# Performance work log

Hardware: AMD Instinct MI355X
Metric: run time of the kernel (lower is better)

Reference implementation:

```python
import jax, jax.numpy as jnp
import numpy as np

B, N, P = 8, 4096, 1024
P4 = P // 4
EPS = 1e-5


def _ln(x, g, b):
    mu = jnp.mean(x, axis=-1, keepdims=True)
    var = jnp.var(x, axis=-1, keepdims=True)
    return (x - mu) * jax.lax.rsqrt(var + EPS) * g + b


def setup_inputs() -> dict:
    key = jax.random.key(0)
    ks = jax.random.split(key, 16)
    s = lambda fan: 1.0 / np.sqrt(fan)
    return {
        "xyz": jax.random.normal(ks[0], (B, N, 3), jnp.float32),
        "x": jax.random.normal(ks[1], (B, N, P), jnp.float32),
        "ln1_g": jnp.ones((P,), jnp.float32),
        "ln1_b": jnp.zeros((P,), jnp.float32),
        "ln2_g": jnp.ones((P,), jnp.float32),
        "ln2_b": jnp.zeros((P,), jnp.float32),
        "qk_w": jax.random.normal(ks[2], (P4, P), jnp.float32) * s(P),   # shared q/k 1x1 conv, no bias
        "v_w": jax.random.normal(ks[3], (P, P), jnp.float32) * s(P),
        "v_b": jax.random.normal(ks[4], (P,), jnp.float32) * s(P),
        "t1_w": jax.random.normal(ks[5], (P, P4), jnp.float32) * s(P4),  # trans_conv
        "t1_b": jax.random.normal(ks[6], (P,), jnp.float32) * s(P4),
        "t2_w": jax.random.normal(ks[7], (P, P4), jnp.float32) * s(P4),  # trans_conv1
        "t2_b": jax.random.normal(ks[8], (P,), jnp.float32) * s(P4),
        "m1_w": jax.random.normal(ks[9], (P, P), jnp.float32) * s(P),
        "m1_b": jax.random.normal(ks[10], (P,), jnp.float32) * s(P),
        "m2_w": jax.random.normal(ks[11], (P, P), jnp.float32) * s(P),
        "m2_b": jax.random.normal(ks[12], (P,), jnp.float32) * s(P),
    }


def reference(xyz, x, ln1_g, ln1_b, ln2_g, ln2_b, qk_w, v_w, v_b,
              t1_w, t1_b, t2_w, t2_b, m1_w, m1_b, m2_w, m2_b):
    # xyz is accepted but unused, matching the torch module. Dropout = eval identity.
    res1 = x
    h = _ln(x, ln1_g, ln1_b)                                   # [B,N,P]
    # TransformerBlock_1 (1x1 convs on h^T [B,P,N] are just matmuls over P)
    x_q = jnp.einsum('op,bnp->bon', qk_w, h)                   # [B,P4,N]
    # k shares weights with q; x_k permuted is x_q transposed
    x_v = jnp.einsum('op,bnp->bno', v_w, h) + v_b              # [B,N,P]
    energy = jnp.einsum('bqn,bkn->bqk', x_q, x_q)              # [B,P4,P4]
    att = jnp.einsum('op,bpk->bok', t1_w, energy) + t1_b[:, None]   # [B,P,P4]
    att = jax.nn.gelu(att, approximate=False)
    att = jnp.einsum('op,bkp->bok', t2_w, att) + t2_b[:, None]      # [B,P,P]
    att = jax.nn.softmax(att, axis=-1)
    t_out = jnp.einsum('bnp,bpq->bnq', x_v, att)               # [B,N,P]
    x1 = t_out + res1
    h2 = _ln(x1, ln2_g, ln2_b)
    m = jax.nn.gelu(h2 @ m1_w.T + m1_b, approximate=False)
    m = m @ m2_w.T + m2_b
    return x1 + m
```

## Files before the change

### kernel.cpp

```cpp
#include <hip/hip_runtime.h>


typedef __attribute__((ext_vector_type(4))) float f32x4;
typedef __attribute__((ext_vector_type(8))) _Float16 h16x8;
typedef __attribute__((ext_vector_type(8))) unsigned short u16x8;
typedef __attribute__((ext_vector_type(4))) unsigned short u16x4;

__device__ __forceinline__ unsigned short f2h(float f) {
  _Float16 h = (_Float16)f;
  return __builtin_bit_cast(unsigned short, h);
}
__device__ __forceinline__ unsigned split16(float f) {
  _Float16 h = (_Float16)f;
  _Float16 l = (_Float16)(f - (float)h);
  return (unsigned)__builtin_bit_cast(unsigned short, h) |
         ((unsigned)__builtin_bit_cast(unsigned short, l) << 16);
}
__device__ __forceinline__ float gelu_f(float x) {
  return 0.5f * x * (1.0f + erff(x * 0.70710678118654752f));
}
__device__ __forceinline__ void gload16(const void* g, void* l) {
  __builtin_amdgcn_global_load_lds(
      (const __attribute__((address_space(1))) unsigned int*)g,
      (__attribute__((address_space(3))) unsigned int*)l, 16, 0, 0);
}

__global__ __launch_bounds__(256)
void ln_kernel(const float* __restrict__ x, const float* __restrict__ g,
               const float* __restrict__ b, unsigned short* __restrict__ hi,
               unsigned short* __restrict__ lo) {
  __shared__ float red[16];
  const size_t base = (size_t)blockIdx.x * 1024;
  const int t = threadIdx.x;
  f32x4 v = *(const f32x4*)&x[base + t * 4];
  float s = v[0] + v[1] + v[2] + v[3];
  float q = v[0] * v[0] + v[1] * v[1] + v[2] * v[2] + v[3] * v[3];
#pragma unroll
  for (int o = 32; o > 0; o >>= 1) { s += __shfl_down(s, o); q += __shfl_down(q, o); }
  const int w = t >> 6;
  if ((t & 63) == 0) { red[w] = s; red[8 + w] = q; }
  __syncthreads();
  s = (red[0] + red[1]) + (red[2] + red[3]);
  q = (red[8] + red[9]) + (red[10] + red[11]);
  const float mu = s * (1.0f / 1024.0f);
  const float var = q * (1.0f / 1024.0f) - mu * mu;
  const float is = rsqrtf(var + 1e-5f);
  f32x4 gg = *(const f32x4*)&g[t * 4];
  f32x4 bb = *(const f32x4*)&b[t * 4];
  u16x4 oh, ol;
#pragma unroll
  for (int j = 0; j < 4; j++) {
    float y = (v[j] - mu) * is * gg[j] + bb[j];
    unsigned p = split16(y);
    oh[j] = (unsigned short)(p & 0xffffu);
    ol[j] = (unsigned short)(p >> 16);
  }
  *(u16x4*)&hi[base + t * 4] = oh;
  if (lo) *(u16x4*)&lo[base + t * 4] = ol;
}

__global__ __launch_bounds__(256)
void cvt_kernel(const float* __restrict__ in, unsigned short* __restrict__ hi,
                unsigned short* __restrict__ lo, int n4) {
  int i = blockIdx.x * 256 + threadIdx.x;
  if (i < n4) {
    f32x4 v = *(const f32x4*)&in[(size_t)i * 4];
    u16x4 oh, ol;
#pragma unroll
    for (int j = 0; j < 4; j++) {
      unsigned p = split16(v[j]);
      oh[j] = (unsigned short)(p & 0xffffu);
      ol[j] = (unsigned short)(p >> 16);
    }
    *(u16x4*)&hi[(size_t)i * 4] = oh;
    if (lo) *(u16x4*)&lo[(size_t)i * 4] = ol;
  }
}

template <int EPI, int SPLIT>
__global__ __launch_bounds__(256)
void gemm16(const unsigned short* __restrict__ Ahi, const unsigned short* __restrict__ Alo,
            const unsigned short* __restrict__ Bhi, const unsigned short* __restrict__ Blo,
            void* __restrict__ Cout, unsigned short* __restrict__ Cout2,
            const float* __restrict__ bias, const float* __restrict__ resIn,
            int K, int lda, int ldb, int ldc,
            long long sA, long long sB, long long sC, long long sRes, int splitK) {
  __shared__ short As[16384];
  __shared__ short Bs[16384];
  const int z = blockIdx.z;
  const int bi = z / splitK, sp = z % splitK;
  const int kLen = K / splitK, kStart = sp * kLen;
  const unsigned short* AH = Ahi + (size_t)bi * sA;
  const unsigned short* BH = Bhi + (size_t)bi * sB;
  const unsigned short* AL = SPLIT ? Alo + (size_t)bi * sA : nullptr;
  const unsigned short* BL = SPLIT ? Blo + (size_t)bi * sB : nullptr;

  int bx = blockIdx.x, by = blockIdx.y;
  {
    const int nwg = gridDim.x * gridDim.y;
    if ((nwg & 7) == 0 && nwg >= 16) {
      const int flat = bx + gridDim.x * by;
      const int chunk = nwg >> 3;
      const int nf = (flat & 7) * chunk + (flat >> 3);
      bx = nf % gridDim.x;
      by = nf / gridDim.x;
    }
  }
  const int mBase = by * 128, nBase = bx * 128;
  const int t = threadIdx.x, w = t >> 6, l = t & 63;
  const int r16 = l & 15, kq = l >> 4;
  const int wr = (w >> 1) * 64, wc = (w & 1) * 64;
  f32x4 acc[4][4] = {};

  auto stage_hi = [&](int buf, int k0) {
#pragma unroll
    for (int it = 0; it < 4; ++it) {
      const int c = it * 256 + t;
      const int row = c >> 3, cc = c & 7;
      const int gc = cc ^ (row & 7);
      const int cbase = it * 256 + w * 64;
      gload16(&AH[(size_t)(mBase + row) * lda + k0 + gc * 8], &As[buf * 8192 + cbase * 8]);
      gload16(&BH[(size_t)(nBase + row) * ldb + k0 + gc * 8], &Bs[buf * 8192 + cbase * 8]);
    }
  };

  if constexpr (!SPLIT) {
    const int nt = kLen >> 6;
    stage_hi(0, kStart);
    asm volatile("s_waitcnt vmcnt(0)" ::: "memory");
    __syncthreads();
    int cur = 0;
    for (int ts = 0; ts < nt; ++ts) {
      if (ts + 1 < nt) stage_hi(cur ^ 1, kStart + (ts + 1) * 64);
#pragma unroll
      for (int kk = 0; kk < 2; ++kk) {
        h16x8 aH[4], bH[4];
#pragma unroll
        for (int mi = 0; mi < 4; mi++) {
          const int r = wr + mi * 16 + r16;
          const int cc = (kk * 4 + kq) ^ (r & 7);
          aH[mi] = *(const h16x8*)&As[cur * 8192 + r * 64 + cc * 8];
        }
#pragma unroll
        for (int ni = 0; ni < 4; ni++) {
          const int r = wc + ni * 16 + r16;
          const int cc = (kk * 4 + kq) ^ (r & 7);
          bH[ni] = *(const h16x8*)&Bs[cur * 8192 + r * 64 + cc * 8];
        }
#pragma unroll
        for (int mi = 0; mi < 4; mi++)
#pragma unroll
          for (int ni = 0; ni < 4; ni++)
            acc[mi][ni] = __builtin_amdgcn_mfma_f32_16x16x32_f16(aH[mi], bH[ni], acc[mi][ni], 0, 0, 0);
      }
      asm volatile("s_waitcnt vmcnt(0)" ::: "memory");
      __syncthreads();
      cur ^= 1;
    }
  } else {
    for (int k0 = kStart; k0 < kStart + kLen; k0 += 64) {
#pragma unroll
      for (int it = 0; it < 4; ++it) {
        const int c = it * 256 + t;
        const int row = c >> 3, cc = c & 7;
        const int gc = cc ^ (row & 7);
        const int cbase = it * 256 + w * 64;
        const size_t ga = (size_t)(mBase + row) * lda + k0 + gc * 8;
        const size_t gb = (size_t)(nBase + row) * ldb + k0 + gc * 8;
        gload16(&AH[ga], &As[cbase * 8]);
        gload16(&BH[gb], &Bs[cbase * 8]);
        gload16(&AL[ga], &As[8192 + cbase * 8]);
        gload16(&BL[gb], &Bs[8192 + cbase * 8]);
      }
      asm volatile("s_waitcnt vmcnt(0)" ::: "memory");
      __syncthreads();
#pragma unroll
      for (int kk = 0; kk < 2; ++kk) {
        h16x8 aH[4], bH[4], aL[4], bL[4];
#pragma unroll
        for (int mi = 0; mi < 4; mi++) {
          const int r = wr + mi * 16 + r16;
          const int cc = (kk * 4 + kq) ^ (r & 7);
          aH[mi] = *(const h16x8*)&As[r * 64 + cc * 8];
          aL[mi] = *(const h16x8*)&As[8192 + r * 64 + cc * 8];
        }
#pragma unroll
        for (int ni = 0; ni < 4; ni++) {
          const int r = wc + ni * 16 + r16;
          const int cc = (kk * 4 + kq) ^ (r & 7);
          bH[ni] = *(const h16x8*)&Bs[r * 64 + cc * 8];
          bL[ni] = *(const h16x8*)&Bs[8192 + r * 64 + cc * 8];
        }
#pragma unroll
        for (int mi = 0; mi < 4; mi++)
#pragma unroll
          for (int ni = 0; ni < 4; ni++) {
            acc[mi][ni] = __builtin_amdgcn_mfma_f32_16x16x32_f16(aH[mi], bH[ni], acc[mi][ni], 0, 0, 0);
            acc[mi][ni] = __builtin_amdgcn_mfma_f32_16x16x32_f16(aH[mi], bL[ni], acc[mi][ni], 0, 0, 0);
            acc[mi][ni] = __builtin_amdgcn_mfma_f32_16x16x32_f16(aL[mi], bH[ni], acc[mi][ni], 0, 0, 0);
          }
      }
      __syncthreads();
    }
  }

  unsigned short* C16 = (unsigned short*)Cout + (size_t)z * sC;
  unsigned short* C16b = Cout2 ? Cout2 + (size_t)z * sC : nullptr;
  float* C32 = (float*)Cout + (size_t)z * sC;
  const float* res = (EPI == 2 || EPI == 3) ? (resIn + (size_t)z * sRes) : nullptr;
#pragma unroll
  for (int mi = 0; mi < 4; mi++) {
#pragma unroll
    for (int ni = 0; ni < 4; ni++) {
      const int cl = nBase + wc + ni * 16 + r16;
      float bcol = 0.0f;
      if (EPI == 0 || EPI == 1 || EPI == 3) bcol = bias[cl];
#pragma unroll
      for (int r = 0; r < 4; r++) {
        const int rw = mBase + wr + mi * 16 + kq * 4 + r;
        float v = acc[mi][ni][r] + bcol;
        if (EPI == 6 || EPI == 7) v += bias[rw];
        if (EPI == 1 || EPI == 6) v = gelu_f(v);
        if (EPI == 2 || EPI == 3) v += res[(size_t)rw * ldc + cl];
        const size_t idx = (size_t)rw * ldc + cl;
        if (EPI == 0 || EPI == 1) C16[idx] = f2h(v);
        else if (EPI == 4 || EPI == 6) {
          unsigned p = split16(v);
          C16[idx] = (unsigned short)(p & 0xffffu);
          C16b[idx] = (unsigned short)(p >> 16);
        }
        else C32[idx] = v;
      }
    }
  }
}

__global__ __launch_bounds__(256)
void ereduce_kernel(const float* __restrict__ part, unsigned short* __restrict__ ehi,
                    unsigned short* __restrict__ elo) {
  const size_t idx = (size_t)blockIdx.x * 256 + threadIdx.x;
  const size_t b = idx >> 16, i = idx & 65535;
  const float* p = part + b * (8ull * 65536) + i;
  float s0 = (p[0] + p[65536]) + (p[2 * 65536] + p[3 * 65536]);
  float s1 = (p[4 * 65536] + p[5 * 65536]) + (p[6 * 65536] + p[7 * 65536]);
  unsigned pk = split16(s0 + s1);
  ehi[idx] = (unsigned short)(pk & 0xffffu);
  elo[idx] = (unsigned short)(pk >> 16);
}

__global__ __launch_bounds__(256)
void smax_t_kernel(const float* __restrict__ a2, unsigned short* __restrict__ attT) {
  __shared__ float S[8][1028];
  __shared__ float inv[8];
  const int t = threadIdx.x;
  const int b = blockIdx.y;
  const int o0 = blockIdx.x * 8;
  const float* src = a2 + ((size_t)b * 1024 + o0) * 1024;
#pragma unroll
  for (int i = 0; i < 8; i++)
    *(f32x4*)&S[i][t * 4] = *(const f32x4*)&src[(size_t)i * 1024 + t * 4];
  __syncthreads();
  const int w = t >> 6, l = t & 63;
  for (int rr = 0; rr < 2; rr++) {
    const int r = w * 2 + rr;
    float m = -1e30f;
#pragma unroll
    for (int i = 0; i < 16; i++) m = fmaxf(m, S[r][l + i * 64]);
#pragma unroll
    for (int o = 32; o > 0; o >>= 1) m = fmaxf(m, __shfl_xor(m, o));
    float ssum = 0.0f;
#pragma unroll
    for (int i = 0; i < 16; i++) {
      float e = expf(S[r][l + i * 64] - m);
      S[r][l + i * 64] = e;
      ssum += e;
    }
#pragma unroll
    for (int o = 32; o > 0; o >>= 1) ssum += __shfl_xor(ssum, o);
    if (l == 0) inv[r] = 1.0f / ssum;
  }
  __syncthreads();
  float iv[8];
#pragma unroll
  for (int r = 0; r < 8; r++) iv[r] = inv[r];
#pragma unroll
  for (int i = 0; i < 4; i++) {
    const int k = i * 256 + t;
    u16x8 ov;
#pragma unroll
    for (int r = 0; r < 8; r++) ov[r] = f2h(S[r][k] * iv[r]);
    *(u16x8*)&attT[((size_t)b * 1024 + k) * 1024 + o0] = ov;
  }
}

extern "C" void kernel_launch(void* const* d_in, const int* in_sizes, int n_in,
                              void* d_out, int out_size, void* d_ws, size_t ws_size,
                              hipStream_t stream) {
  (void)in_sizes; (void)n_in; (void)out_size; (void)ws_size;
  const float* x     = (const float*)d_in[1];
  const float* ln1_g = (const float*)d_in[2];
  const float* ln1_b = (const float*)d_in[3];
  const float* ln2_g = (const float*)d_in[4];
  const float* ln2_b = (const float*)d_in[5];
  const float* qk_w  = (const float*)d_in[6];
  const float* v_w   = (const float*)d_in[7];
  const float* v_b   = (const float*)d_in[8];
  const float* t1_w  = (const float*)d_in[9];
  const float* t1_b  = (const float*)d_in[10];
  const float* t2_w  = (const float*)d_in[11];
  const float* t2_b  = (const float*)d_in[12];
  const float* m1_w  = (const float*)d_in[13];
  const float* m1_b  = (const float*)d_in[14];
  const float* m2_w  = (const float*)d_in[15];
  const float* m2_b  = (const float*)d_in[16];

  char* ws = (char*)d_ws;
  unsigned short* hhi  = (unsigned short*)(ws + 0);
  unsigned short* hlo  = (unsigned short*)(ws + 67108864);
  unsigned short* Qthi = (unsigned short*)(ws + 134217728);
  unsigned short* Qtlo = (unsigned short*)(ws + 150994944);
  float*          part = (float*)(ws + 167772160);
  unsigned short* Ehi  = (unsigned short*)(ws + 184549376);
  unsigned short* Elo  = (unsigned short*)(ws + 185597952);
  unsigned short* Ghi  = (unsigned short*)(ws + 186646528);
  unsigned short* Glo  = (unsigned short*)(ws + 190840832);
  float*          a2   = (float*)(ws + 195035136);
  unsigned short* attT = (unsigned short*)(ws + 228589568);
  unsigned short* xv   = (unsigned short*)(ws + 245366784);
  float*          x1   = (float*)(ws + 312475648);
  unsigned short* wqh  = (unsigned short*)(ws + 446693376);
  unsigned short* wql  = (unsigned short*)(ws + 447217664);
  unsigned short* wv   = (unsigned short*)(ws + 447741952);
  unsigned short* wt1h = (unsigned short*)(ws + 449839104);
  unsigned short* wt1l = (unsigned short*)(ws + 450363392);
  unsigned short* wt2h = (unsigned short*)(ws + 450887680);
  unsigned short* wt2l = (unsigned short*)(ws + 451411968);
  unsigned short* wm1  = (unsigned short*)(ws + 451936256);
  unsigned short* wm2  = (unsigned short*)(ws + 454033408);
  unsigned short* h2 = hhi;
  unsigned short* gb = hlo;
  float* out = (float*)d_out;

  cvt_kernel<<<dim3(256),  dim3(256), 0, stream>>>(qk_w, wqh, wql, 65536);
  cvt_kernel<<<dim3(1024), dim3(256), 0, stream>>>(v_w, wv, nullptr, 262144);
  cvt_kernel<<<dim3(256),  dim3(256), 0, stream>>>(t1_w, wt1h, wt1l, 65536);
  cvt_kernel<<<dim3(256),  dim3(256), 0, stream>>>(t2_w, wt2h, wt2l, 65536);
  cvt_kernel<<<dim3(1024), dim3(256), 0, stream>>>(m1_w, wm1, nullptr, 262144);
  cvt_kernel<<<dim3(1024), dim3(256), 0, stream>>>(m2_w, wm2, nullptr, 262144);
  ln_kernel<<<dim3(32768), dim3(256), 0, stream>>>(x, ln1_g, ln1_b, hhi, hlo);
  gemm16<4, 1><<<dim3(32, 2, 8), dim3(256), 0, stream>>>(
      wqh, wql, hhi, hlo, Qthi, Qtlo, nullptr, nullptr,
      1024, 1024, 1024, 4096, 0, 4194304, 1048576, 0, 1);
  gemm16<0, 0><<<dim3(8, 256, 1), dim3(256), 0, stream>>>(
      hhi, nullptr, wv, nullptr, xv, nullptr, v_b, nullptr,
      1024, 1024, 1024, 1024, 0, 0, 0, 0, 1);
  gemm16<5, 1><<<dim3(2, 2, 64), dim3(256), 0, stream>>>(
      Qthi, Qtlo, Qthi, Qtlo, part, nullptr, nullptr, nullptr,
      4096, 4096, 4096, 256, 1048576, 1048576, 65536, 0, 8);
  ereduce_kernel<<<dim3(2048), dim3(256), 0, stream>>>(part, Ehi, Elo);
  gemm16<6, 1><<<dim3(2, 8, 8), dim3(256), 0, stream>>>(
      wt1h, wt1l, Ehi, Elo, Ghi, Glo, t1_b, nullptr,
      256, 256, 256, 256, 0, 65536, 262144, 0, 1);
  gemm16<7, 1><<<dim3(8, 8, 8), dim3(256), 0, stream>>>(
      wt2h, wt2l, Ghi, Glo, a2, nullptr, t2_b, nullptr,
      256, 256, 256, 1024, 0, 262144, 1048576, 0, 1);
  smax_t_kernel<<<dim3(128, 8), dim3(256), 0, stream>>>(a2, attT);
  gemm16<2, 0><<<dim3(8, 32, 8), dim3(256), 0, stream>>>(
      xv, nullptr, attT, nullptr, x1, nullptr, nullptr, x,
      1024, 1024, 1024, 1024, 4194304, 1048576, 4194304, 4194304, 1);
  ln_kernel<<<dim3(32768), dim3(256), 0, stream>>>(x1, ln2_g, ln2_b, h2, nullptr);
  gemm16<1, 0><<<dim3(8, 256, 1), dim3(256), 0, stream>>>(
      h2, nullptr, wm1, nullptr, gb, nullptr, m1_b, nullptr,
      1024, 1024, 1024, 1024, 0, 0, 0, 0, 1);
  gemm16<3, 0><<<dim3(8, 256, 1), dim3(256), 0, stream>>>(
      gb, nullptr, wm2, nullptr, out, nullptr, m2_b, x1,
      1024, 1024, 1024, 1024, 0, 0, 0, 0, 1);
}
```

Measured before the change: 733.5 us.

## Split GEMM into 256x256-tile fp16 kernel and double-buffered split-precision kernel

```diff
diff --git a/kernel.cpp b/kernel.cpp
--- a/kernel.cpp
+++ b/kernel.cpp
@@ -77,24 +77,18 @@
   }
 }
 
-template <int EPI, int SPLIT>
-__global__ __launch_bounds__(256)
-void gemm16(const unsigned short* __restrict__ Ahi, const unsigned short* __restrict__ Alo,
-            const unsigned short* __restrict__ Bhi, const unsigned short* __restrict__ Blo,
-            void* __restrict__ Cout, unsigned short* __restrict__ Cout2,
-            const float* __restrict__ bias, const float* __restrict__ resIn,
+template <int EPI>
+__global__ __launch_bounds__(512)
+void gemm_v(const unsigned short* __restrict__ Ain, const unsigned short* __restrict__ Bin,
+            void* __restrict__ Cout, const float* __restrict__ bias,
+            const float* __restrict__ resIn,
             int K, int lda, int ldb, int ldc,
-            long long sA, long long sB, long long sC, long long sRes, int splitK) {
-  __shared__ short As[16384];
-  __shared__ short Bs[16384];
+            long long sA, long long sB, long long sC, long long sRes) {
+  __shared__ short As[2][16384];
+  __shared__ short Bs[2][16384];
   const int z = blockIdx.z;
-  const int bi = z / splitK, sp = z % splitK;
-  const int kLen = K / splitK, kStart = sp * kLen;
-  const unsigned short* AH = Ahi + (size_t)bi * sA;
-  const unsigned short* BH = Bhi + (size_t)bi * sB;
-  const unsigned short* AL = SPLIT ? Alo + (size_t)bi * sA : nullptr;
-  const unsigned short* BL = SPLIT ? Blo + (size_t)bi * sB : nullptr;
-
+  const unsigned short* A = Ain + (size_t)z * sA;
+  const unsigned short* B = Bin + (size_t)z * sB;
   int bx = blockIdx.x, by = blockIdx.y;
   {
     const int nwg = gridDim.x * gridDim.y;
@@ -106,130 +100,182 @@
       by = nf / gridDim.x;
     }
   }
+  const int mBase = by * 256, nBase = bx * 256;
+  const int t = threadIdx.x, w = t >> 6, l = t & 63;
+  const int r16 = l & 15, kq = l >> 4;
+  const int wr = (w >> 2) * 128, wc = (w & 3) * 64;
+  f32x4 acc[8][4] = {};
+
+  auto stage = [&](int buf, int k0) {
+#pragma unroll
+    for (int i = 0; i < 4; ++i) {
+      const int c = i * 512 + t;
+      const int row = c >> 3, cc = c & 7;
+      const int gc = cc ^ (row & 7);
+      const int cbase = i * 512 + w * 64;
+      gload16(&A[(size_t)(mBase + row) * lda + k0 + gc * 8], &As[buf][cbase * 8]);
+      gload16(&B[(size_t)(nBase + row) * ldb + k0 + gc * 8], &Bs[buf][cbase * 8]);
+    }
+  };
+
+  const int nt = K >> 6;
+  stage(0, 0);
+  asm volatile("s_waitcnt vmcnt(0)" ::: "memory");
+  __syncthreads();
+  for (int ts = 0; ts < nt; ++ts) {
+    const int cur = ts & 1;
+    if (ts + 1 < nt) stage(cur ^ 1, (ts + 1) * 64);
+#pragma unroll
+    for (int kk = 0; kk < 2; ++kk) {
+      h16x8 aF[8], bF[4];
+#pragma unroll
+      for (int ni = 0; ni < 4; ni++) {
+        const int r = wc + ni * 16 + r16;
+        bF[ni] = *(const h16x8*)&Bs[cur][r * 64 + (((kk * 4 + kq) ^ (r & 7))) * 8];
+      }
+#pragma unroll
+      for (int mi = 0; mi < 8; mi++) {
+        const int r = wr + mi * 16 + r16;
+        aF[mi] = *(const h16x8*)&As[cur][r * 64 + (((kk * 4 + kq) ^ (r & 7))) * 8];
+      }
+#pragma unroll
+      for (int mi = 0; mi < 8; mi++)
+#pragma unroll
+        for (int ni = 0; ni < 4; ni++)
+          acc[mi][ni] = __builtin_amdgcn_mfma_f32_16x16x32_f16(aF[mi], bF[ni], acc[mi][ni], 0, 0, 0);
+    }
+    asm volatile("s_waitcnt vmcnt(0)" ::: "memory");
+    __syncthreads();
+  }
+
+  unsigned short* C16 = (unsigned short*)Cout + (size_t)z * sC;
+  float* C32 = (float*)Cout + (size_t)z * sC;
+  const float* res = (EPI >= 2) ? (resIn + (size_t)z * sRes) : nullptr;
+#pragma unroll
+  for (int mi = 0; mi < 8; mi++) {
+#pragma unroll
+    for (int ni = 0; ni < 4; ni++) {
+      const int cl = nBase + wc + ni * 16 + r16;
+      const float bcol = (EPI != 2) ? bias[cl] : 0.0f;
+#pragma unroll
+      for (int r = 0; r < 4; r++) {
+        const int rw = mBase + wr + mi * 16 + kq * 4 + r;
+        float v = acc[mi][ni][r] + bcol;
+        if (EPI == 1) v = gelu_f(v);
+        if (EPI >= 2) v += res[(size_t)rw * ldc + cl];
+        if (EPI <= 1) C16[(size_t)rw * ldc + cl] = f2h(v);
+        else          C32[(size_t)rw * ldc + cl] = v;
+      }
+    }
+  }
+}
+
+template <int EPI>
+__global__ __launch_bounds__(256)
+void gemm_s(const unsigned short* __restrict__ Ahi, const unsigned short* __restrict__ Alo,
+            const unsigned short* __restrict__ Bhi, const unsigned short* __restrict__ Blo,
+            void* __restrict__ Cout, unsigned short* __restrict__ Cout2,
+            const float* __restrict__ bias,
+            int K, int lda, int ldb, int ldc,
+            long long sA, long long sB, long long sC, int splitK) {
+  __shared__ short As[2][8192];
+  __shared__ short Bs[2][8192];
+  const int z = blockIdx.z;
+  const int bi = z / splitK, sp = z % splitK;
+  const int kLen = K / splitK, kStart = sp * kLen;
+  const unsigned short* AH = Ahi + (size_t)bi * sA;
+  const unsigned short* BH = Bhi + (size_t)bi * sB;
+  const unsigned short* AL = Alo + (size_t)bi * sA;
+  const unsigned short* BL = Blo + (size_t)bi * sB;
+  int bx = blockIdx.x, by = blockIdx.y;
+  {
+    const int nwg = gridDim.x * gridDim.y;
+    if ((nwg & 7) == 0 && nwg >= 16) {
+      const int flat = bx + gridDim.x * by;
+      const int chunk = nwg >> 3;
+      const int nf = (flat & 7) * chunk + (flat >> 3);
+      bx = nf % gridDim.x;
+      by = nf / gridDim.x;
+    }
+  }
   const int mBase = by * 128, nBase = bx * 128;
   const int t = threadIdx.x, w = t >> 6, l = t & 63;
   const int r16 = l & 15, kq = l >> 4;
   const int wr = (w >> 1) * 64, wc = (w & 1) * 64;
   f32x4 acc[4][4] = {};
 
-  auto stage_hi = [&](int buf, int k0) {
-#pragma unroll
-    for (int it = 0; it < 4; ++it) {
-      const int c = it * 256 + t;
-      const int row = c >> 3, cc = c & 7;
-      const int gc = cc ^ (row & 7);
-      const int cbase = it * 256 + w * 64;
-      gload16(&AH[(size_t)(mBase + row) * lda + k0 + gc * 8], &As[buf * 8192 + cbase * 8]);
-      gload16(&BH[(size_t)(nBase + row) * ldb + k0 + gc * 8], &Bs[buf * 8192 + cbase * 8]);
+  auto stage = [&](int buf, int k0) {
+#pragma unroll
+    for (int i = 0; i < 2; ++i) {
+      const int c = i * 256 + t;
+      const int row = c >> 2, cc = c & 3;
+      const int gc = cc ^ ((row >> 1) & 3);
+      const int cbase = i * 256 + w * 64;
+      const size_t ga = (size_t)(mBase + row) * lda + k0 + gc * 8;
+      const size_t gb = (size_t)(nBase + row) * ldb + k0 + gc * 8;
+      gload16(&AH[ga], &As[buf][cbase * 8]);
+      gload16(&AL[ga], &As[buf][4096 + cbase * 8]);
+      gload16(&BH[gb], &Bs[buf][cbase * 8]);
+      gload16(&BL[gb], &Bs[buf][4096 + cbase * 8]);
     }
   };
 
-  if constexpr (!SPLIT) {
-    const int nt = kLen >> 6;
-    stage_hi(0, kStart);
+  const int nsteps = kLen >> 5;
+  stage(0, kStart);
+  asm volatile("s_waitcnt vmcnt(0)" ::: "memory");
+  __syncthreads();
+  for (int ts = 0; ts < nsteps; ++ts) {
+    const int cur = ts & 1;
+    if (ts + 1 < nsteps) stage(cur ^ 1, kStart + (ts + 1) * 32);
+    h16x8 aH[4], bH[4], aL[4], bL[4];
+#pragma unroll
+    for (int mi = 0; mi < 4; mi++) {
+      const int r = wr + mi * 16 + r16;
+      const int off = r * 32 + (kq ^ ((r >> 1) & 3)) * 8;
+      aH[mi] = *(const h16x8*)&As[cur][off];
+      aL[mi] = *(const h16x8*)&As[cur][4096 + off];
+    }
+#pragma unroll
+    for (int ni = 0; ni < 4; ni++) {
+      const int r = wc + ni * 16 + r16;
+      const int off = r * 32 + (kq ^ ((r >> 1) & 3)) * 8;
+      bH[ni] = *(const h16x8*)&Bs[cur][off];
+      bL[ni] = *(const h16x8*)&Bs[cur][4096 + off];
+    }
+#pragma unroll
+    for (int mi = 0; mi < 4; mi++)
+#pragma unroll
+      for (int ni = 0; ni < 4; ni++) {
+        acc[mi][ni] = __builtin_amdgcn_mfma_f32_16x16x32_f16(aH[mi], bH[ni], acc[mi][ni], 0, 0, 0);
+        acc[mi][ni] = __builtin_amdgcn_mfma_f32_16x16x32_f16(aH[mi], bL[ni], acc[mi][ni], 0, 0, 0);
+        acc[mi][ni] = __builtin_amdgcn_mfma_f32_16x16x32_f16(aL[mi], bH[ni], acc[mi][ni], 0, 0, 0);
+      }
     asm volatile("s_waitcnt vmcnt(0)" ::: "memory");
     __syncthreads();
-    int cur = 0;
-    for (int ts = 0; ts < nt; ++ts) {
-      if (ts + 1 < nt) stage_hi(cur ^ 1, kStart + (ts + 1) * 64);
-#pragma unroll
-      for (int kk = 0; kk < 2; ++kk) {
-        h16x8 aH[4], bH[4];
-#pragma unroll
-        for (int mi = 0; mi < 4; mi++) {
-          const int r = wr + mi * 16 + r16;
-          const int cc = (kk * 4 + kq) ^ (r & 7);
-          aH[mi] = *(const h16x8*)&As[cur * 8192 + r * 64 + cc * 8];
-        }
-#pragma unroll
-        for (int ni = 0; ni < 4; ni++) {
-          const int r = wc + ni * 16 + r16;
-          const int cc = (kk * 4 + kq) ^ (r & 7);
-          bH[ni] = *(const h16x8*)&Bs[cur * 8192 + r * 64 + cc * 8];
-        }
-#pragma unroll
-        for (int mi = 0; mi < 4; mi++)
-#pragma unroll
-          for (int ni = 0; ni < 4; ni++)
-            acc[mi][ni] = __builtin_amdgcn_mfma_f32_16x16x32_f16(aH[mi], bH[ni], acc[mi][ni], 0, 0, 0);
-      }
-      asm volatile("s_waitcnt vmcnt(0)" ::: "memory");
-      __syncthreads();
-      cur ^= 1;
-    }
-  } else {
-    for (int k0 = kStart; k0 < kStart + kLen; k0 += 64) {
-#pragma unroll
-      for (int it = 0; it < 4; ++it) {
-        const int c = it * 256 + t;
-        const int row = c >> 3, cc = c & 7;
-        const int gc = cc ^ (row & 7);
-        const int cbase = it * 256 + w * 64;
-        const size_t ga = (size_t)(mBase + row) * lda + k0 + gc * 8;
-        const size_t gb = (size_t)(nBase + row) * ldb + k0 + gc * 8;
-        gload16(&AH[ga], &As[cbase * 8]);
-        gload16(&BH[gb], &Bs[cbase * 8]);
-        gload16(&AL[ga], &As[8192 + cbase * 8]);
-        gload16(&BL[gb], &Bs[8192 + cbase * 8]);
-      }
-      asm volatile("s_waitcnt vmcnt(0)" ::: "memory");
-      __syncthreads();
-#pragma unroll
-      for (int kk = 0; kk < 2; ++kk) {
-        h16x8 aH[4], bH[4], aL[4], bL[4];
-#pragma unroll
-        for (int mi = 0; mi < 4; mi++) {
-          const int r = wr + mi * 16 + r16;
-          const int cc = (kk * 4 + kq) ^ (r & 7);
-          aH[mi] = *(const h16x8*)&As[r * 64 + cc * 8];
-          aL[mi] = *(const h16x8*)&As[8192 + r * 64 + cc * 8];
-        }
-#pragma unroll
-        for (int ni = 0; ni < 4; ni++) {
-          const int r = wc + ni * 16 + r16;
-          const int cc = (kk * 4 + kq) ^ (r & 7);
-          bH[ni] = *(const h16x8*)&Bs[r * 64 + cc * 8];
-          bL[ni] = *(const h16x8*)&Bs[8192 + r * 64 + cc * 8];
-        }
-#pragma unroll
-        for (int mi = 0; mi < 4; mi++)
-#pragma unroll
-          for (int ni = 0; ni < 4; ni++) {
-            acc[mi][ni] = __builtin_amdgcn_mfma_f32_16x16x32_f16(aH[mi], bH[ni], acc[mi][ni], 0, 0, 0);
-            acc[mi][ni] = __builtin_amdgcn_mfma_f32_16x16x32_f16(aH[mi], bL[ni], acc[mi][ni], 0, 0, 0);
-            acc[mi][ni] = __builtin_amdgcn_mfma_f32_16x16x32_f16(aL[mi], bH[ni], acc[mi][ni], 0, 0, 0);
-          }
-      }
-      __syncthreads();
-    }
   }
 
   unsigned short* C16 = (unsigned short*)Cout + (size_t)z * sC;
   unsigned short* C16b = Cout2 ? Cout2 + (size_t)z * sC : nullptr;
   float* C32 = (float*)Cout + (size_t)z * sC;
-  const float* res = (EPI == 2 || EPI == 3) ? (resIn + (size_t)z * sRes) : nullptr;
 #pragma unroll
   for (int mi = 0; mi < 4; mi++) {
 #pragma unroll
     for (int ni = 0; ni < 4; ni++) {
       const int cl = nBase + wc + ni * 16 + r16;
-      float bcol = 0.0f;
-      if (EPI == 0 || EPI == 1 || EPI == 3) bcol = bias[cl];
 #pragma unroll
       for (int r = 0; r < 4; r++) {
         const int rw = mBase + wr + mi * 16 + kq * 4 + r;
-        float v = acc[mi][ni][r] + bcol;
+        float v = acc[mi][ni][r];
         if (EPI == 6 || EPI == 7) v += bias[rw];
-        if (EPI == 1 || EPI == 6) v = gelu_f(v);
-        if (EPI == 2 || EPI == 3) v += res[(size_t)rw * ldc + cl];
+        if (EPI == 6) v = gelu_f(v);
         const size_t idx = (size_t)rw * ldc + cl;
-        if (EPI == 0 || EPI == 1) C16[idx] = f2h(v);
-        else if (EPI == 4 || EPI == 6) {
+        if (EPI == 4 || EPI == 6) {
           unsigned p = split16(v);
           C16[idx] = (unsigned short)(p & 0xffffu);
           C16b[idx] = (unsigned short)(p >> 16);
+        } else {
+          C32[idx] = v;
         }
-        else C32[idx] = v;
       }
     }
   }
@@ -348,31 +394,27 @@
   cvt_kernel<<<dim3(1024), dim3(256), 0, stream>>>(m1_w, wm1, nullptr, 262144);
   cvt_kernel<<<dim3(1024), dim3(256), 0, stream>>>(m2_w, wm2, nullptr, 262144);
   ln_kernel<<<dim3(32768), dim3(256), 0, stream>>>(x, ln1_g, ln1_b, hhi, hlo);
-  gemm16<4, 1><<<dim3(32, 2, 8), dim3(256), 0, stream>>>(
-      wqh, wql, hhi, hlo, Qthi, Qtlo, nullptr, nullptr,
-      1024, 1024, 1024, 4096, 0, 4194304, 1048576, 0, 1);
-  gemm16<0, 0><<<dim3(8, 256, 1), dim3(256), 0, stream>>>(
-      hhi, nullptr, wv, nullptr, xv, nullptr, v_b, nullptr,
-      1024, 1024, 1024, 1024, 0, 0, 0, 0, 1);
-  gemm16<5, 1><<<dim3(2, 2, 64), dim3(256), 0, stream>>>(
-      Qthi, Qtlo, Qthi, Qtlo, part, nullptr, nullptr, nullptr,
-      4096, 4096, 4096, 256, 1048576, 1048576, 65536, 0, 8);
+  gemm_s<4><<<dim3(32, 2, 8), dim3(256), 0, stream>>>(
+      wqh, wql, hhi, hlo, Qthi, Qtlo, nullptr,
+      1024, 1024, 1024, 4096, 0, 4194304, 1048576, 1);
+  gemm_v<0><<<dim3(4, 128, 1), dim3(512), 0, stream>>>(
+      hhi, wv, xv, v_b, nullptr, 1024, 1024, 1024, 1024, 0, 0, 0, 0);
+  gemm_s<5><<<dim3(2, 2, 64), dim3(256), 0, stream>>>(
+      Qthi, Qtlo, Qthi, Qtlo, part, nullptr, nullptr,
+      4096, 4096, 4096, 256, 1048576, 1048576, 65536, 8);
   ereduce_kernel<<<dim3(2048), dim3(256), 0, stream>>>(part, Ehi, Elo);
-  gemm16<6, 1><<<dim3(2, 8, 8), dim3(256), 0, stream>>>(
-      wt1h, wt1l, Ehi, Elo, Ghi, Glo, t1_b, nullptr,
-      256, 256, 256, 256, 0, 65536, 262144, 0, 1);
-  gemm16<7, 1><<<dim3(8, 8, 8), dim3(256), 0, stream>>>(
-      wt2h, wt2l, Ghi, Glo, a2, nullptr, t2_b, nullptr,
-      256, 256, 256, 1024, 0, 262144, 1048576, 0, 1);
+  gemm_s<6><<<dim3(2, 8, 8), dim3(256), 0, stream>>>(
+      wt1h, wt1l, Ehi, Elo, Ghi, Glo, t1_b,
+      256, 256, 256, 256, 0, 65536, 262144, 1);
+  gemm_s<7><<<dim3(8, 8, 8), dim3(256), 0, stream>>>(
+      wt2h, wt2l, Ghi, Glo, a2, nullptr, t2_b,
+      256, 256, 256, 1024, 0, 262144, 1048576, 1);
   smax_t_kernel<<<dim3(128, 8), dim3(256), 0, stream>>>(a2, attT);
-  gemm16<2, 0><<<dim3(8, 32, 8), dim3(256), 0, stream>>>(
-      xv, nullptr, attT, nullptr, x1, nullptr, nullptr, x,
-      1024, 1024, 1024, 1024, 4194304, 1048576, 4194304, 4194304, 1);
+  gemm_v<2><<<dim3(4, 16, 8), dim3(512), 0, stream>>>(
+      xv, attT, x1, nullptr, x, 1024, 1024, 1024, 1024, 4194304, 1048576, 4194304, 4194304);
   ln_kernel<<<dim3(32768), dim3(256), 0, stream>>>(x1, ln2_g, ln2_b, h2, nullptr);
-  gemm16<1, 0><<<dim3(8, 256, 1), dim3(256), 0, stream>>>(
-      h2, nullptr, wm1, nullptr, gb, nullptr, m1_b, nullptr,
-      1024, 1024, 1024, 1024, 0, 0, 0, 0, 1);
-  gemm16<3, 0><<<dim3(8, 256, 1), dim3(256), 0, stream>>>(
-      gb, nullptr, wm2, nullptr, out, nullptr, m2_b, x1,
-      1024, 1024, 1024, 1024, 0, 0, 0, 0, 1);
-}
+  gemm_v<1><<<dim3(4, 128, 1), dim3(512), 0, stream>>>(
+      h2, wm1, gb, m1_b, nullptr, 1024, 1024, 1024, 1024, 0, 0, 0, 0);
+  gemm_v<3><<<dim3(4, 128, 1), dim3(512), 0, stream>>>(
+      gb, wm2, out, m2_b, x1, 1024, 1024, 1024, 1024, 0, 0, 0, 0);
+}
```

After: 732.3 us. Within noise of the previous version (-0.2%).
